# Kernel tuning notes

Hardware: AMD Instinct MI355X
Metric: run time of the kernel (lower is better)

## Reference

```python
import jax, jax.numpy as jnp
import numpy as np

B_, H_, N_, L_ = 4, 512, 64, 2048  # batch, d_model, d_state/2 (conj pairs), seq len


def setup_inputs() -> dict:
    key = jax.random.key(0)
    ks = jax.random.split(key, 8)
    x = jax.random.normal(ks[0], (B_, H_, L_), jnp.float32)
    ln_w = jnp.ones((H_,), jnp.float32)
    ln_b = jnp.zeros((H_,), jnp.float32)
    # S4D-style init: dt log-uniform in [1e-3, 1e-1], A = -1/2 + i*pi*n (S4D-Lin)
    log_dt = jax.random.uniform(ks[1], (H_,), jnp.float32) * (np.log(0.1) - np.log(0.001)) + np.log(0.001)
    log_A_real = jnp.broadcast_to(jnp.log(jnp.float32(0.5)), (H_, N_))
    A_imag = jnp.broadcast_to(np.pi * jnp.arange(N_, dtype=np.float32), (H_, N_))
    B_re = jnp.ones((H_, N_), jnp.float32)
    B_im = jnp.zeros((H_, N_), jnp.float32)
    # 2 kernel channels for bidirectional
    C_re = jax.random.normal(ks[2], (2, H_, N_), jnp.float32) * (0.5 ** 0.5)
    C_im = jax.random.normal(ks[3], (2, H_, N_), jnp.float32) * (0.5 ** 0.5)
    D = jax.random.normal(ks[4], (H_,), jnp.float32)
    W_out = jax.random.normal(ks[5], (H_, H_), jnp.float32) / np.sqrt(H_)
    b_out = jnp.zeros((H_,), jnp.float32)
    return dict(x=x, ln_w=ln_w, ln_b=ln_b, log_dt=log_dt, log_A_real=log_A_real,
                A_imag=A_imag, B_re=B_re, B_im=B_im, C_re=C_re, C_im=C_im,
                D=D, W_out=W_out, b_out=b_out)


def _s4_layer(x, ln_w, ln_b, log_dt, log_A_real, A_imag, B_re, B_im, C_re, C_im, D, W_out, b_out):
    Bb, H, L = x.shape
    # ---- pre-norm LayerNorm over channel dim (module transposes to (B,L,H)) ----
    zt = x.transpose(0, 2, 1)                          # (B, L, H)
    mu = zt.mean(-1, keepdims=True)
    var = jnp.mean((zt - mu) ** 2, -1, keepdims=True)
    zt = (zt - mu) * jax.lax.rsqrt(var + 1e-5) * ln_w + ln_b
    z = zt.transpose(0, 2, 1)                          # (B, H, L)
    # ---- S4 diagonal SSM kernel, ZOH discretization, 2 channels (bidirectional) ----
    dt = jnp.exp(log_dt)[:, None]                      # (H, 1)
    A = -jnp.exp(log_A_real) + 1j * A_imag             # (H, N)
    dtA = A * dt                                       # (H, N)
    dB = (B_re + 1j * B_im) * (jnp.exp(dtA) - 1.0) / A # (H, N) discretized B
    CB = (C_re + 1j * C_im) * dB                       # (2, H, N)
    V = jnp.exp(dtA[:, :, None] * jnp.arange(L))       # (H, N, L) Vandermonde exp(l*dt*A)
    k = 2.0 * jnp.real(jnp.einsum('chn,hnl->chl', CB, V))  # (2, H, L)
    # ---- bidirectional: causal + flipped anticausal kernel, length 2L ----
    zpad = jnp.zeros_like(k[0])
    kb = jnp.concatenate([k[0], zpad], -1) + jnp.concatenate([zpad, k[1][:, ::-1]], -1)  # (H, 2L)
    # ---- FFT convolution ----
    k_f = jnp.fft.rfft(kb, n=2 * L)                    # (H, L+1)
    u_f = jnp.fft.rfft(z, n=2 * L)                     # (B, H, L+1)
    y = jnp.fft.irfft(u_f * k_f, n=2 * L)[..., :L]     # (B, H, L)
    y = y + z * D[:, None]                             # skip connection D*u
    y = jax.nn.gelu(y)                                 # default S4 activation
    y = jnp.einsum('oh,bhl->bol', W_out, y) + b_out[:, None]  # output linear (Conv1d k=1)
    return y + x                                       # residual of S4Layer


def reference(x, ln_w, ln_b, log_dt, log_A_real, A_imag, B_re, B_im, C_re, C_im, D, W_out, b_out):
    return _s4_layer(x, ln_w, ln_b, log_dt, log_A_real, A_imag, B_re, B_im, C_re, C_im, D, W_out, b_out)
```

## Files before the change

kernel.cpp:

```cpp
#include <hip/hip_runtime.h>
#include <math.h>

#define Bq 4
#define Hq 512
#define Nq 64
#define Lq 2048
#define PARAM (Hq*Nq)
#define T 64
#define NC (Lq/T)
#define NCOL 256

__global__ void prep_kernel(const float* __restrict__ log_dt,
                            const float* __restrict__ log_A_real,
                            const float* __restrict__ A_imag,
                            const float* __restrict__ B_re, const float* __restrict__ B_im,
                            const float* __restrict__ C_re, const float* __restrict__ C_im,
                            float* __restrict__ a0, float* __restrict__ b0,
                            float* __restrict__ a1, float* __restrict__ b1,
                            float* __restrict__ pw) {
    int idx = blockIdx.x * blockDim.x + threadIdx.x;
    if (idx >= PARAM) return;
    int h = idx >> 6, n = idx & 63;
    float dt = expf(log_dt[h]);
    float Ar = -expf(log_A_real[idx]);
    float Ai = A_imag[idx];
    float er = expf(Ar * dt);
    float wr = er * cosf(Ai * dt);
    float wi = er * sinf(Ai * dt);
    float mr = wr - 1.0f, mi = wi;
    float den = Ar * Ar + Ai * Ai;
    float qr = (mr * Ar + mi * Ai) / den;
    float qi = (mi * Ar - mr * Ai) / den;
    float Br = B_re[idx], Bi = B_im[idx];
    float dBr = Br * qr - Bi * qi;
    float dBi = Br * qi + Bi * qr;
    float cr = C_re[idx], ci = C_im[idx];
    a0[idx] =  2.0f * (cr * dBr - ci * dBi);
    b0[idx] = -2.0f * (cr * dBi + ci * dBr);
    cr = C_re[PARAM + idx]; ci = C_im[PARAM + idx];
    a1[idx] =  2.0f * (cr * dBr - ci * dBi);
    b1[idx] = -2.0f * (cr * dBi + ci * dBr);
    float c = 1.f, s = 0.f;
    float* base = pw + (size_t)h * 65 * 128 + 2 * n;
    for (int d = 0; d <= 64; ++d) {
        *(float2*)(base + (size_t)d * 128) = float2{c, s};
        float nc = c * wr - s * wi;
        float ns = c * wi + s * wr;
        c = nc; s = ns;
    }
}

__global__ __launch_bounds__(128)
void ktap_kernel(const float* __restrict__ pw,
                 const float* __restrict__ a0, const float* __restrict__ b0,
                 const float* __restrict__ a1, const float* __restrict__ b1,
                 float* __restrict__ kt) {
    int h = blockIdx.x;
    int t = threadIdx.x;
    int dir = t >> 6, d = t & 63;
    const float* aa = dir ? a1 : a0;
    const float* bb = dir ? b1 : b0;
    const float* row = pw + (size_t)(h * 65 + d) * 128;
    float acc = 0.f;
    for (int n = 0; n < 64; ++n) {
        float2 v = *(const float2*)(row + 2 * n);
        acc = fmaf(aa[h * 64 + n], v.x, acc);
        acc = fmaf(bb[h * 64 + n], v.y, acc);
    }
    kt[((size_t)h * 2 + dir) * 64 + d] = acc;
}

__global__ __launch_bounds__(256)
void ln_kernel(const float* __restrict__ x, const float* __restrict__ lnw,
               const float* __restrict__ lnb, float* __restrict__ z) {
    int blk = blockIdx.x;
    int b  = blk / (Lq / 16);
    int l0 = (blk % (Lq / 16)) * 16;
    int tx = threadIdx.x & 15;
    int ty = threadIdx.x >> 4;
    const float* xb = x + (size_t)b * Hq * Lq;
    float s = 0.f, s2 = 0.f;
    for (int h = ty; h < Hq; h += 16) {
        float v = xb[h * Lq + l0 + tx];
        s += v; s2 += v * v;
    }
    __shared__ float rs_[16][17], r2_[16][17], mu_s[16], sg_s[16];
    rs_[ty][tx] = s; r2_[ty][tx] = s2;
    __syncthreads();
    if (ty == 0) {
        float a = 0.f, c = 0.f;
        #pragma unroll
        for (int i = 0; i < 16; ++i) { a += rs_[i][tx]; c += r2_[i][tx]; }
        float mu = a * (1.0f / Hq);
        float var = c * (1.0f / Hq) - mu * mu;
        mu_s[tx] = mu;
        sg_s[tx] = rsqrtf(var + 1e-5f);
    }
    __syncthreads();
    float mu = mu_s[tx], rs = sg_s[tx];
    float* zb = z + (size_t)b * Hq * Lq;
    for (int h = ty; h < Hq; h += 16) {
        float v = xb[h * Lq + l0 + tx];
        zb[h * Lq + l0 + tx] = (v - mu) * rs * lnw[h] + lnb[h];
    }
}


__global__ __launch_bounds__(256, 6)
void delta_kernel(const float* __restrict__ z, const float* __restrict__ pw,
                  float* __restrict__ buf) {
    __shared__ float Bs[64][68];
    int h = blockIdx.x, ct = blockIdx.y;
    int t = threadIdx.x;
    int dir = ct >> 1;
    int cc = t & 31, rb = (t >> 5) & 1, jg = t >> 6;
    int b = (ct & 1) * 2 + rb;
    const float* zb = z + ((size_t)b * Hq + h) * Lq;
    if (dir == 0) {
        #pragma unroll
        for (int f = 0; f < 4; ++f) {
            float4 v = *(const float4*)(zb + cc * 64 + 16 * jg + 4 * f);
            Bs[16*jg+4*f+0][rb*32+cc] = v.x;
            Bs[16*jg+4*f+1][rb*32+cc] = v.y;
            Bs[16*jg+4*f+2][rb*32+cc] = v.z;
            Bs[16*jg+4*f+3][rb*32+cc] = v.w;
        }
    } else {
        #pragma unroll
        for (int f = 0; f < 4; ++f) {
            float4 v = *(const float4*)(zb + 2044 - cc * 64 - 16 * jg - 4 * f);
            Bs[16*jg+4*f+3][rb*32+cc] = v.x;
            Bs[16*jg+4*f+2][rb*32+cc] = v.y;
            Bs[16*jg+4*f+1][rb*32+cc] = v.z;
            Bs[16*jg+4*f+0][rb*32+cc] = v.w;
        }
    }
    __syncthreads();
    int tx = t & 15, ty = t >> 4;
    float aR[4][4] = {}, aI[4][4] = {};
    const float* pwh = pw + (size_t)h * 65 * 128;
    #pragma unroll 4
    for (int kk = 0; kk < 64; ++kk) {
        int d = 63 - kk;
        const float4* pr = (const float4*)(pwh + (size_t)d * 128 + 8 * tx);
        float4 p0 = pr[0], p1 = pr[1];
        float4 bv = *(const float4*)&Bs[kk][4 * ty];
        float pc[4] = {p0.x, p0.z, p1.x, p1.z};
        float ps[4] = {p0.y, p0.w, p1.y, p1.w};
        #pragma unroll
        for (int rr = 0; rr < 4; ++rr) {
            #pragma unroll
            for (int q = 0; q < 4; ++q) {
                aR[rr][q] = fmaf(pc[rr], (&bv.x)[q], aR[rr][q]);
                aI[rr][q] = fmaf(ps[rr], (&bv.x)[q], aI[rr][q]);
            }
        }
    }
    #pragma unroll
    for (int q = 0; q < 4; ++q) {
        int colg = ct * 64 + 4 * ty + q;
        float* dst = buf + ((size_t)h * NCOL + colg) * 128 + 8 * tx;
        float4 v1, v2;
        v1.x = aR[0][q]; v1.y = aI[0][q]; v1.z = aR[1][q]; v1.w = aI[1][q];
        v2.x = aR[2][q]; v2.y = aI[2][q]; v2.z = aR[3][q]; v2.w = aI[3][q];
        *(float4*)dst = v1; *(float4*)(dst + 4) = v2;
    }
}

__global__ __launch_bounds__(256)
void cscan_kernel(const float* __restrict__ pw, float* __restrict__ buf) {
    int e = blockIdx.x * 4 + (threadIdx.x >> 6);
    int n = threadIdx.x & 63;
    int h = e >> 3, dir = (e >> 2) & 1, b = e & 3;
    float2 t64 = *(const float2*)(pw + (size_t)(h * 65 + 64) * 128 + 2 * n);
    float tc = t64.x, ts = t64.y;
    float sr = 0.f, si = 0.f;
    float2* p = (float2*)(buf + ((size_t)h * NCOL + dir * 128 + b * 32) * 128) + n;
    float2 d = p[0];
    for (int c = 0; c < NC; ++c) {
        float2 dn;
        if (c + 1 < NC) dn = p[(c + 1) * 64];
        float2 s; s.x = sr; s.y = si;
        p[c * 64] = s;
        float nr = fmaf(tc, sr, fmaf(-ts, si, d.x));
        float ni = fmaf(ts, sr, fmaf(tc, si, d.y));
        sr = nr; si = ni; d = dn;
    }
}

__global__ __launch_bounds__(256, 8)
void y_kernel(const float* __restrict__ z, const float* __restrict__ pw,
              const float* __restrict__ a0, const float* __restrict__ b0,
              const float* __restrict__ a1, const float* __restrict__ b1,
              const float* __restrict__ kt, const float* __restrict__ buf,
              float* __restrict__ y0, float* __restrict__ y1) {
    __shared__ float As[32][68];
    __shared__ float Bs[32][68];
    __shared__ float ks[64], as_[64], bs_[64];
    int h = blockIdx.x, dir = blockIdx.y, ct = blockIdx.z;
    int t = threadIdx.x;
    if (t < 64) {
        ks[t]  = kt[((size_t)h * 2 + dir) * 64 + t];
        as_[t] = (dir ? a1 : a0)[h * 64 + t];
        bs_[t] = (dir ? b1 : b0)[h * 64 + t];
    }
    int tx = t & 15, ty = t >> 4;
    int si = t & 63, sg = t >> 6;
    int cc = t & 31, rb = (t >> 5) & 1, kg = t >> 6;
    int b = ct * 2 + rb;
    const float* zb = z + ((size_t)b * Hq + h) * Lq;
    int off = (dir == 0) ? 1 : 0;
    const float* prow = pw + (size_t)(h * 65 + si + off) * 128;
    float acc[4][4] = {};
    __syncthreads();
    for (int p = 0; p < 6; ++p) {
        if (p < 2) {
            #pragma unroll
            for (int q = 0; q < 8; ++q) {
                int kk = 8 * sg + q;
                int j = 32 * p + kk;
                int idx = (dir == 0) ? (si - j) : (si - j - 1);
                As[kk][si] = (idx >= 0) ? ks[idx] : 0.f;
            }
        } else {
            #pragma unroll
            for (int q = 0; q < 8; ++q) {
                int kk = 8 * sg + q;
                int m = 32 * (p - 2) + kk;
                int n = m >> 1;
                float2 v = *(const float2*)(prow + 2 * n);
                float av = as_[n], bv = bs_[n];
                As[kk][si] = ((m & 1) == 0) ? fmaf(av, v.x, bv * v.y)
                                            : fmaf(bv, v.x, -av * v.y);
            }
        }
        if (p < 2) {
            if (dir == 0) {
                #pragma unroll
                for (int f = 0; f < 2; ++f) {
                    float4 v = *(const float4*)(zb + cc * 64 + 32 * p + 8 * kg + 4 * f);
                    Bs[8*kg+4*f+0][rb*32+cc] = v.x;
                    Bs[8*kg+4*f+1][rb*32+cc] = v.y;
                    Bs[8*kg+4*f+2][rb*32+cc] = v.z;
                    Bs[8*kg+4*f+3][rb*32+cc] = v.w;
                }
            } else {
                #pragma unroll
                for (int f = 0; f < 2; ++f) {
                    float4 v = *(const float4*)(zb + 2044 - cc * 64 - 32 * p - 8 * kg - 4 * f);
                    Bs[8*kg+4*f+3][rb*32+cc] = v.x;
                    Bs[8*kg+4*f+2][rb*32+cc] = v.y;
                    Bs[8*kg+4*f+1][rb*32+cc] = v.z;
                    Bs[8*kg+4*f+0][rb*32+cc] = v.w;
                }
            }
        } else {
            int colg = dir * 128 + ct * 64 + rb * 32 + cc;
            const float* src = buf + ((size_t)h * NCOL + colg) * 128 + 32 * (p - 2) + 8 * kg;
            float4 v0 = *(const float4*)src;
            float4 v1 = *(const float4*)(src + 4);
            #pragma unroll
            for (int e2 = 0; e2 < 4; ++e2) Bs[8*kg+e2][rb*32+cc]   = (&v0.x)[e2];
            #pragma unroll
            for (int e2 = 0; e2 < 4; ++e2) Bs[8*kg+4+e2][rb*32+cc] = (&v1.x)[e2];
        }
        __syncthreads();
        #pragma unroll 8
        for (int kk = 0; kk < 32; ++kk) {
            float4 av = *(const float4*)&As[kk][4 * tx];
            float4 bv = *(const float4*)&Bs[kk][4 * ty];
            #pragma unroll
            for (int ii = 0; ii < 4; ++ii) {
                float a = (&av.x)[ii];
                acc[ii][0] = fmaf(a, bv.x, acc[ii][0]);
                acc[ii][1] = fmaf(a, bv.y, acc[ii][1]);
                acc[ii][2] = fmaf(a, bv.z, acc[ii][2]);
                acc[ii][3] = fmaf(a, bv.w, acc[ii][3]);
            }
        }
        __syncthreads();
    }
    #pragma unroll
    for (int q = 0; q < 4; ++q) {
        int coll = 4 * ty + q;
        int bo = ct * 2 + (coll >> 5), c = coll & 31;
        float4 v;
        if (dir == 0) {
            v.x = acc[0][q]; v.y = acc[1][q]; v.z = acc[2][q]; v.w = acc[3][q];
            *(float4*)(y0 + ((size_t)bo * Hq + h) * Lq + c * 64 + 4 * tx) = v;
        } else {
            v.x = acc[3][q]; v.y = acc[2][q]; v.z = acc[1][q]; v.w = acc[0][q];
            *(float4*)(y1 + ((size_t)bo * Hq + h) * Lq + 2044 - c * 64 - 4 * tx) = v;
        }
    }
}

__global__ __launch_bounds__(256)
void act_kernel(float4* __restrict__ y0, const float4* __restrict__ y1,
                const float4* __restrict__ z, const float* __restrict__ D) {
    int i4 = blockIdx.x * 256 + threadIdx.x;
    int h = (i4 >> 9) & (Hq - 1);
    float d = D[h];
    float4 v0 = y0[i4], v1 = y1[i4], vz = z[i4];
    float vv[4] = { v0.x + v1.x + d * vz.x, v0.y + v1.y + d * vz.y,
                    v0.z + v1.z + d * vz.z, v0.w + v1.w + d * vz.w };
    #pragma unroll
    for (int i = 0; i < 4; ++i) {
        float v = vv[i];
        float tt = tanhf(0.7978845608028654f * (v + 0.044715f * v * v * v));
        vv[i] = 0.5f * v * (1.0f + tt);
    }
    float4 r; r.x = vv[0]; r.y = vv[1]; r.z = vv[2]; r.w = vv[3];
    y0[i4] = r;
}

__global__ __launch_bounds__(256)
void gemm_kernel(const float* __restrict__ u, const float* __restrict__ W,
                 const float* __restrict__ bias, const float* __restrict__ x,
                 float* __restrict__ out) {
    int l0 = blockIdx.x * 64;
    int o0 = blockIdx.y * 128;
    int b  = blockIdx.z;
    int tid = threadIdx.x;
    __shared__ float Ws[16][129];
    __shared__ float Us[16][65];
    const float* ub = u + (size_t)b * Hq * Lq;
    float acc[8][4] = {};
    int wo = tid >> 4, wl = tid & 15;
    for (int k0 = 0; k0 < Hq; k0 += 16) {
        {
            int j  = tid & 15;
            int ib = tid >> 4;
            #pragma unroll
            for (int r = 0; r < 8; ++r) {
                int i = ib + 16 * r;
                Ws[j][i] = W[(size_t)(o0 + i) * Hq + k0 + j];
            }
            int li = tid & 63;
            int jb = tid >> 6;
            #pragma unroll
            for (int r = 0; r < 4; ++r) {
                int j2 = jb + 4 * r;
                Us[j2][li] = ub[(size_t)(k0 + j2) * Lq + l0 + li];
            }
        }
        __syncthreads();
        #pragma unroll
        for (int j = 0; j < 16; ++j) {
            float av[8], bv[4];
            #pragma unroll
            for (int i = 0; i < 8; ++i) av[i] = Ws[j][8 * wo + i];
            #pragma unroll
            for (int i = 0; i < 4; ++i) bv[i] = Us[j][4 * wl + i];
            #pragma unroll
            for (int io = 0; io < 8; ++io)
                #pragma unroll
                for (int il = 0; il < 4; ++il)
                    acc[io][il] = fmaf(av[io], bv[il], acc[io][il]);
        }
        __syncthreads();
    }
    #pragma unroll
    for (int io = 0; io < 8; ++io) {
        int o = o0 + 8 * wo + io;
        float bo = bias[o];
        size_t base = ((size_t)b * Hq + o) * Lq + l0 + 4 * wl;
        const float4 xr = *(const float4*)(x + base);
        float4 r;
        r.x = acc[io][0] + bo + xr.x;
        r.y = acc[io][1] + bo + xr.y;
        r.z = acc[io][2] + bo + xr.z;
        r.w = acc[io][3] + bo + xr.w;
        *(float4*)(out + base) = r;
    }
}

extern "C" void kernel_launch(void* const* d_in, const int* in_sizes, int n_in,
                              void* d_out, int out_size, void* d_ws, size_t ws_size,
                              hipStream_t stream) {
    (void)in_sizes; (void)n_in; (void)out_size; (void)ws_size;
    const float* x          = (const float*)d_in[0];
    const float* ln_w       = (const float*)d_in[1];
    const float* ln_b       = (const float*)d_in[2];
    const float* log_dt     = (const float*)d_in[3];
    const float* log_A_real = (const float*)d_in[4];
    const float* A_imag     = (const float*)d_in[5];
    const float* B_re       = (const float*)d_in[6];
    const float* B_im       = (const float*)d_in[7];
    const float* C_re       = (const float*)d_in[8];
    const float* C_im       = (const float*)d_in[9];
    const float* Dv         = (const float*)d_in[10];
    const float* W          = (const float*)d_in[11];
    const float* b_out      = (const float*)d_in[12];
    float* out = (float*)d_out;
    float* ws  = (float*)d_ws;

    const size_t BHL = (size_t)Bq * Hq * Lq;
    float* a0  = ws;
    float* b0  = ws + (size_t)PARAM;
    float* a1  = ws + 2 * (size_t)PARAM;
    float* b1  = ws + 3 * (size_t)PARAM;
    float* kt  = ws + 4 * (size_t)PARAM;
    float* pw  = ws + 6 * (size_t)PARAM;
    float* z   = ws + 136 * (size_t)PARAM;
    float* y0  = z  + BHL;
    float* y1  = y0 + BHL;
    float* buf = y1 + BHL;

    prep_kernel<<<PARAM / 256, 256, 0, stream>>>(log_dt, log_A_real, A_imag,
                                                 B_re, B_im, C_re, C_im,
                                                 a0, b0, a1, b1, pw);
    ln_kernel<<<Bq * (Lq / 16), 256, 0, stream>>>(x, ln_w, ln_b, z);
    ktap_kernel<<<Hq, 128, 0, stream>>>(pw, a0, b0, a1, b1, kt);
    delta_kernel<<<dim3(Hq, 4), 256, 0, stream>>>(z, pw, buf);
    cscan_kernel<<<Bq * Hq * 2 / 4, 256, 0, stream>>>(pw, buf);
    y_kernel<<<dim3(Hq, 2, 2), 256, 0, stream>>>(z, pw, a0, b0, a1, b1,
                                                 kt, buf, y0, y1);
    act_kernel<<<(Bq * Hq * Lq / 4) / 256, 256, 0, stream>>>((float4*)y0, (const float4*)y1,
                                                             (const float4*)z, Dv);
    gemm_kernel<<<dim3(Lq / 64, Hq / 128, Bq), 256, 0, stream>>>(y0, W, b_out, x, out);
}
```

Before: 331.8 us.

## Fuse both directions with skip and GELU; double-buffer output GEMM

The per-direction y kernel and the separate activation kernel are merged into one kernel. It computes the causal and anticausal contributions in the same block, reverses the anticausal tile through shared memory, and applies D-skip plus GELU before writing u. This removes the y0/y1 intermediate round trip through global memory and one kernel launch. In exchange the grid shrinks to half as many blocks, each doing twice the work. The output GEMM moves to 512 threads with 32-wide K tiles and register-staged double-buffered shared memory, so global loads overlap compute, but each thread now holds fewer accumulators.

```diff
diff --git a/kernel.cpp b/kernel.cpp
--- a/kernel.cpp
+++ b/kernel.cpp
@@ -105,7 +105,6 @@
     }
 }
 
-
 __global__ __launch_bounds__(256, 6)
 void delta_kernel(const float* __restrict__ z, const float* __restrict__ pw,
                   float* __restrict__ buf) {
@@ -188,38 +187,28 @@
     }
 }
 
-__global__ __launch_bounds__(256, 8)
-void y_kernel(const float* __restrict__ z, const float* __restrict__ pw,
-              const float* __restrict__ a0, const float* __restrict__ b0,
-              const float* __restrict__ a1, const float* __restrict__ b1,
-              const float* __restrict__ kt, const float* __restrict__ buf,
-              float* __restrict__ y0, float* __restrict__ y1) {
-    __shared__ float As[32][68];
-    __shared__ float Bs[32][68];
-    __shared__ float ks[64], as_[64], bs_[64];
-    int h = blockIdx.x, dir = blockIdx.y, ct = blockIdx.z;
-    int t = threadIdx.x;
-    if (t < 64) {
-        ks[t]  = kt[((size_t)h * 2 + dir) * 64 + t];
-        as_[t] = (dir ? a1 : a0)[h * 64 + t];
-        bs_[t] = (dir ? b1 : b0)[h * 64 + t];
-    }
+template <int DIR>
+__device__ __forceinline__ void y_phases(const float* __restrict__ zb0,
+                                         const float* __restrict__ zb1,
+                                         const float* __restrict__ pwh,
+                                         const float* __restrict__ bufh,
+                                         const float* __restrict__ ks,
+                                         const float* __restrict__ as_,
+                                         const float* __restrict__ bs_,
+                                         float (*As)[68], float (*Bs)[68],
+                                         int t, int ctB, float acc[4][4]) {
     int tx = t & 15, ty = t >> 4;
     int si = t & 63, sg = t >> 6;
     int cc = t & 31, rb = (t >> 5) & 1, kg = t >> 6;
-    int b = ct * 2 + rb;
-    const float* zb = z + ((size_t)b * Hq + h) * Lq;
-    int off = (dir == 0) ? 1 : 0;
-    const float* prow = pw + (size_t)(h * 65 + si + off) * 128;
-    float acc[4][4] = {};
-    __syncthreads();
+    const float* zb = rb ? zb1 : zb0;
+    const float* prow = pwh + (size_t)(si + ((DIR == 0) ? 1 : 0)) * 128;
     for (int p = 0; p < 6; ++p) {
         if (p < 2) {
             #pragma unroll
             for (int q = 0; q < 8; ++q) {
                 int kk = 8 * sg + q;
                 int j = 32 * p + kk;
-                int idx = (dir == 0) ? (si - j) : (si - j - 1);
+                int idx = (DIR == 0) ? (si - j) : (si - j - 1);
                 As[kk][si] = (idx >= 0) ? ks[idx] : 0.f;
             }
         } else {
@@ -235,7 +224,7 @@
             }
         }
         if (p < 2) {
-            if (dir == 0) {
+            if (DIR == 0) {
                 #pragma unroll
                 for (int f = 0; f < 2; ++f) {
                     float4 v = *(const float4*)(zb + cc * 64 + 32 * p + 8 * kg + 4 * f);
@@ -255,8 +244,8 @@
                 }
             }
         } else {
-            int colg = dir * 128 + ct * 64 + rb * 32 + cc;
-            const float* src = buf + ((size_t)h * NCOL + colg) * 128 + 32 * (p - 2) + 8 * kg;
+            int colg = DIR * 128 + ctB * 64 + rb * 32 + cc;
+            const float* src = bufh + (size_t)colg * 128 + 32 * (p - 2) + 8 * kg;
             float4 v0 = *(const float4*)src;
             float4 v1 = *(const float4*)(src + 4);
             #pragma unroll
@@ -280,41 +269,70 @@
         }
         __syncthreads();
     }
+}
+
+__global__ __launch_bounds__(256, 4)
+void yact_kernel(const float* __restrict__ z, const float* __restrict__ pw,
+                 const float* __restrict__ a0, const float* __restrict__ b0,
+                 const float* __restrict__ a1, const float* __restrict__ b1,
+                 const float* __restrict__ kt, const float* __restrict__ buf,
+                 const float* __restrict__ Dv, float* __restrict__ u) {
+    __shared__ float sh[64 * 68];
+    __shared__ float ks0[64], ks1[64], as0[64], bs0[64], as1[64], bs1[64];
+    int h = blockIdx.x, ctB = blockIdx.y;
+    int t = threadIdx.x;
+    if (t < 64) {
+        ks0[t] = kt[((size_t)h * 2 + 0) * 64 + t];
+        ks1[t] = kt[((size_t)h * 2 + 1) * 64 + t];
+        as0[t] = a0[h * 64 + t]; bs0[t] = b0[h * 64 + t];
+        as1[t] = a1[h * 64 + t]; bs1[t] = b1[h * 64 + t];
+    }
+    __syncthreads();
+    const float* zb0 = z + ((size_t)(2 * ctB) * Hq + h) * Lq;
+    const float* zb1 = z + ((size_t)(2 * ctB + 1) * Hq + h) * Lq;
+    const float* pwh = pw + (size_t)h * 65 * 128;
+    const float* bufh = buf + (size_t)h * NCOL * 128;
+    float (*As)[68] = (float(*)[68])sh;
+    float (*Bs)[68] = (float(*)[68])(sh + 32 * 68);
+    float acc0[4][4] = {}, acc1[4][4] = {};
+    y_phases<0>(zb0, zb1, pwh, bufh, ks0, as0, bs0, As, Bs, t, ctB, acc0);
+    y_phases<1>(zb0, zb1, pwh, bufh, ks1, as1, bs1, As, Bs, t, ctB, acc1);
+    float (*S1)[68] = (float(*)[68])sh;
+    int tx = t & 15, ty = t >> 4;
+    #pragma unroll
+    for (int q = 0; q < 4; ++q) {
+        float4 v;
+        v.x = acc1[0][q]; v.y = acc1[1][q]; v.z = acc1[2][q]; v.w = acc1[3][q];
+        *(float4*)&S1[4 * ty + q][4 * tx] = v;
+    }
+    __syncthreads();
+    float dv = Dv[h];
     #pragma unroll
     for (int q = 0; q < 4; ++q) {
         int coll = 4 * ty + q;
-        int bo = ct * 2 + (coll >> 5), c = coll & 31;
-        float4 v;
-        if (dir == 0) {
-            v.x = acc[0][q]; v.y = acc[1][q]; v.z = acc[2][q]; v.w = acc[3][q];
-            *(float4*)(y0 + ((size_t)bo * Hq + h) * Lq + c * 64 + 4 * tx) = v;
-        } else {
-            v.x = acc[3][q]; v.y = acc[2][q]; v.z = acc[1][q]; v.w = acc[0][q];
-            *(float4*)(y1 + ((size_t)bo * Hq + h) * Lq + 2044 - c * 64 - 4 * tx) = v;
-        }
-    }
-}
-
-__global__ __launch_bounds__(256)
-void act_kernel(float4* __restrict__ y0, const float4* __restrict__ y1,
-                const float4* __restrict__ z, const float* __restrict__ D) {
-    int i4 = blockIdx.x * 256 + threadIdx.x;
-    int h = (i4 >> 9) & (Hq - 1);
-    float d = D[h];
-    float4 v0 = y0[i4], v1 = y1[i4], vz = z[i4];
-    float vv[4] = { v0.x + v1.x + d * vz.x, v0.y + v1.y + d * vz.y,
-                    v0.z + v1.z + d * vz.z, v0.w + v1.w + d * vz.w };
-    #pragma unroll
-    for (int i = 0; i < 4; ++i) {
-        float v = vv[i];
-        float tt = tanhf(0.7978845608028654f * (v + 0.044715f * v * v * v));
-        vv[i] = 0.5f * v * (1.0f + tt);
-    }
-    float4 r; r.x = vv[0]; r.y = vv[1]; r.z = vv[2]; r.w = vv[3];
-    y0[i4] = r;
-}
-
-__global__ __launch_bounds__(256)
+        int rb2 = coll >> 5, cc2 = coll & 31;
+        int b = 2 * ctB + rb2;
+        int colrev = rb2 * 32 + (31 - cc2);
+        float4 w = *(const float4*)&S1[colrev][60 - 4 * tx];
+        size_t base = ((size_t)b * Hq + h) * Lq + cc2 * 64 + 4 * tx;
+        float4 zr = *(const float4*)(z + base);
+        float vv[4];
+        vv[0] = acc0[0][q] + w.w + dv * zr.x;
+        vv[1] = acc0[1][q] + w.z + dv * zr.y;
+        vv[2] = acc0[2][q] + w.y + dv * zr.z;
+        vv[3] = acc0[3][q] + w.x + dv * zr.w;
+        #pragma unroll
+        for (int i = 0; i < 4; ++i) {
+            float v = vv[i];
+            float tt = tanhf(0.7978845608028654f * (v + 0.044715f * v * v * v));
+            vv[i] = 0.5f * v * (1.0f + tt);
+        }
+        float4 r; r.x = vv[0]; r.y = vv[1]; r.z = vv[2]; r.w = vv[3];
+        *(float4*)(u + base) = r;
+    }
+}
+
+__global__ __launch_bounds__(512, 4)
 void gemm_kernel(const float* __restrict__ u, const float* __restrict__ W,
                  const float* __restrict__ bias, const float* __restrict__ x,
                  float* __restrict__ out) {
@@ -322,47 +340,59 @@
     int o0 = blockIdx.y * 128;
     int b  = blockIdx.z;
     int tid = threadIdx.x;
-    __shared__ float Ws[16][129];
-    __shared__ float Us[16][65];
+    __shared__ float Ws[2][32][132];
+    __shared__ float Us[2][32][68];
     const float* ub = u + (size_t)b * Hq * Lq;
-    float acc[8][4] = {};
+    float acc[4][4] = {};
     int wo = tid >> 4, wl = tid & 15;
-    for (int k0 = 0; k0 < Hq; k0 += 16) {
-        {
-            int j  = tid & 15;
-            int ib = tid >> 4;
-            #pragma unroll
-            for (int r = 0; r < 8; ++r) {
-                int i = ib + 16 * r;
-                Ws[j][i] = W[(size_t)(o0 + i) * Hq + k0 + j];
-            }
-            int li = tid & 63;
-            int jb = tid >> 6;
-            #pragma unroll
-            for (int r = 0; r < 4; ++r) {
-                int j2 = jb + 4 * r;
-                Us[j2][li] = ub[(size_t)(k0 + j2) * Lq + l0 + li];
-            }
+    int sj = tid & 31, so = tid >> 5;
+    int sl = tid & 63, sk = tid >> 6;
+    float wreg[8], ureg[4];
+    #pragma unroll
+    for (int r = 0; r < 8; ++r) wreg[r] = W[(size_t)(o0 + so + 16*r) * Hq + sj];
+    #pragma unroll
+    for (int r = 0; r < 4; ++r) ureg[r] = ub[(size_t)(4*sk + r) * Lq + l0 + sl];
+    #pragma unroll
+    for (int r = 0; r < 8; ++r) Ws[0][sj][so + 16*r] = wreg[r];
+    #pragma unroll
+    for (int r = 0; r < 4; ++r) Us[0][4*sk + r][sl] = ureg[r];
+    __syncthreads();
+    for (int t = 0; t < Hq / 32; ++t) {
+        int cur = t & 1;
+        if (t < 15) {
+            int k0 = (t + 1) * 32;
+            #pragma unroll
+            for (int r = 0; r < 8; ++r)
+                wreg[r] = W[(size_t)(o0 + so + 16*r) * Hq + k0 + sj];
+            #pragma unroll
+            for (int r = 0; r < 4; ++r)
+                ureg[r] = ub[(size_t)(k0 + 4*sk + r) * Lq + l0 + sl];
+        }
+        #pragma unroll 8
+        for (int j = 0; j < 32; ++j) {
+            float4 av = *(const float4*)&Ws[cur][j][4 * wo];
+            float4 bv = *(const float4*)&Us[cur][j][4 * wl];
+            #pragma unroll
+            for (int io = 0; io < 4; ++io) {
+                float a = (&av.x)[io];
+                acc[io][0] = fmaf(a, bv.x, acc[io][0]);
+                acc[io][1] = fmaf(a, bv.y, acc[io][1]);
+                acc[io][2] = fmaf(a, bv.z, acc[io][2]);
+                acc[io][3] = fmaf(a, bv.w, acc[io][3]);
+            }
+        }
+        if (t < 15) {
+            int nxt = cur ^ 1;
+            #pragma unroll
+            for (int r = 0; r < 8; ++r) Ws[nxt][sj][so + 16*r] = wreg[r];
+            #pragma unroll
+            for (int r = 0; r < 4; ++r) Us[nxt][4*sk + r][sl] = ureg[r];
         }
         __syncthreads();
-        #pragma unroll
-        for (int j = 0; j < 16; ++j) {
-            float av[8], bv[4];
-            #pragma unroll
-            for (int i = 0; i < 8; ++i) av[i] = Ws[j][8 * wo + i];
-            #pragma unroll
-            for (int i = 0; i < 4; ++i) bv[i] = Us[j][4 * wl + i];
-            #pragma unroll
-            for (int io = 0; io < 8; ++io)
-                #pragma unroll
-                for (int il = 0; il < 4; ++il)
-                    acc[io][il] = fmaf(av[io], bv[il], acc[io][il]);
-        }
-        __syncthreads();
-    }
-    #pragma unroll
-    for (int io = 0; io < 8; ++io) {
-        int o = o0 + 8 * wo + io;
+    }
+    #pragma unroll
+    for (int io = 0; io < 4; ++io) {
+        int o = o0 + 4 * wo + io;
         float bo = bias[o];
         size_t base = ((size_t)b * Hq + o) * Lq + l0 + 4 * wl;
         const float4 xr = *(const float4*)(x + base);
@@ -403,9 +433,8 @@
     float* kt  = ws + 4 * (size_t)PARAM;
     float* pw  = ws + 6 * (size_t)PARAM;
     float* z   = ws + 136 * (size_t)PARAM;
-    float* y0  = z  + BHL;
-    float* y1  = y0 + BHL;
-    float* buf = y1 + BHL;
+    float* u   = z  + BHL;
+    float* buf = u + BHL;
 
     prep_kernel<<<PARAM / 256, 256, 0, stream>>>(log_dt, log_A_real, A_imag,
                                                  B_re, B_im, C_re, C_im,
@@ -414,9 +443,7 @@
     ktap_kernel<<<Hq, 128, 0, stream>>>(pw, a0, b0, a1, b1, kt);
     delta_kernel<<<dim3(Hq, 4), 256, 0, stream>>>(z, pw, buf);
     cscan_kernel<<<Bq * Hq * 2 / 4, 256, 0, stream>>>(pw, buf);
-    y_kernel<<<dim3(Hq, 2, 2), 256, 0, stream>>>(z, pw, a0, b0, a1, b1,
-                                                 kt, buf, y0, y1);
-    act_kernel<<<(Bq * Hq * Lq / 4) / 256, 256, 0, stream>>>((float4*)y0, (const float4*)y1,
-                                                             (const float4*)z, Dv);
-    gemm_kernel<<<dim3(Lq / 64, Hq / 128, Bq), 256, 0, stream>>>(y0, W, b_out, x, out);
-}
+    yact_kernel<<<dim3(Hq, 2), 256, 0, stream>>>(z, pw, a0, b0, a1, b1,
+                                                 kt, buf, Dv, u);
+    gemm_kernel<<<dim3(Lq / 64, Hq / 128, Bq), 512, 0, stream>>>(u, W, b_out, x, out);
+}
```

Result: faster. 308.3 us (-7.1%).
